# Optimization experiments

Hardware: AMD Instinct MI355X
Metric: run time of the kernel (lower is better)

The kernel has to match this reference:

```python
import jax, jax.numpy as jnp
import numpy as np

N, IN_DIM, OUT_DIM, H = 1024, 128, 128, 4
D = OUT_DIM // H  # head_dim = 32
NEG_SLOPE = 0.2
MASK_VAL = -1e9
LN_EPS = 1e-5


def setup_inputs() -> dict:
    key = jax.random.key(0)
    k = jax.random.split(key, 8)
    h = jax.random.normal(k[0], (N, IN_DIM), dtype=jnp.float32)
    adj = jax.random.randint(k[1], (N, N), 0, 2, dtype=jnp.int32)
    adj = adj.at[jnp.arange(N), jnp.arange(N)].set(1)  # self-loops
    s = 1.0 / np.sqrt(IN_DIM)
    W_l = jax.random.normal(k[2], (IN_DIM, OUT_DIM), dtype=jnp.float32) * s
    W_r = jax.random.normal(k[3], (IN_DIM, OUT_DIM), dtype=jnp.float32) * s
    W_v = jax.random.normal(k[4], (IN_DIM, OUT_DIM), dtype=jnp.float32) * s
    a = jax.random.normal(k[5], (D,), dtype=jnp.float32) * (1.0 / np.sqrt(D))
    ln_g = jnp.ones((OUT_DIM,), dtype=jnp.float32)
    ln_b = jnp.zeros((OUT_DIM,), dtype=jnp.float32)
    return {"h": h, "adj": adj, "W_l": W_l, "W_r": W_r, "W_v": W_v,
            "a": a, "ln_g": ln_g, "ln_b": ln_b}


def reference(h, adj, W_l, W_r, W_v, a, ln_g, ln_b):
    n = h.shape[0]
    Wlh = (h @ W_l).reshape(n, H, D)   # [N,H,D]
    Wrh = (h @ W_r).reshape(n, H, D)   # [N,H,D]
    # pairwise additive scores: pair[i,j,h,d] = Wlh[i] + Wrh[j]
    pair = Wlh[:, None, :, :] + Wrh[None, :, :, :]          # [N,N,H,D]
    pair = jnp.where(pair >= 0, pair, NEG_SLOPE * pair)      # leaky_relu(0.2)
    e = jnp.einsum('ijhd,d->ijh', pair, a)                   # [N,N,H]
    mask = (adj != 0)[:, :, None]                            # [N,N,1]
    e = jnp.where(mask, e, MASK_VAL)
    alpha = jax.nn.softmax(e, axis=1)                        # softmax over j
    v = (h @ W_v).reshape(n, H, D)                           # [N,H,D]
    agg = jnp.einsum('ijh,jhd->ihd', alpha, v).reshape(n, OUT_DIM)
    mu = jnp.mean(agg, axis=-1, keepdims=True)
    var = jnp.mean((agg - mu) ** 2, axis=-1, keepdims=True)
    y = (agg - mu) * jax.lax.rsqrt(var + LN_EPS) * ln_g + ln_b
    return jax.nn.relu(y)
```

## Files before the change

kernel.cpp:

```cpp
#include <hip/hip_runtime.h>
#include <cstdint>

typedef _Float16 f16;
typedef _Float16 f16x2 __attribute__((ext_vector_type(2)));
typedef _Float16 f16x4 __attribute__((ext_vector_type(4)));
typedef _Float16 f16x8 __attribute__((ext_vector_type(8)));
typedef float    f32x4 __attribute__((ext_vector_type(4)));
typedef unsigned short u16;
typedef unsigned int   u32;

#define LOG2E 1.44269504088896340736f

__device__ __forceinline__ f16x2 habs2(f16x2 v) {
    union { f16x2 h; u32 u; } x; x.h = v; x.u &= 0x7FFF7FFFu; return x.h;
}
#if __has_builtin(__builtin_amdgcn_fdot2)
__device__ __forceinline__ float fdot2f(f16x2 a, f16x2 b, float c) {
    return __builtin_amdgcn_fdot2(a, b, c, false);
}
#else
__device__ __forceinline__ float fdot2f(f16x2 a, f16x2 b, float c) {
    return c + (float)a.x * (float)b.x + (float)a.y * (float)b.y;
}
#endif
#if __has_builtin(__builtin_amdgcn_exp2f)
#define EXP2F __builtin_amdgcn_exp2f
#else
#define EXP2F exp2f
#endif

__global__ __launch_bounds__(384) void k1_proj(
        const float* __restrict__ Wl, const float* __restrict__ Wr,
        const float* __restrict__ Wv, const float* __restrict__ h,
        const float* __restrict__ a_,
        f16* __restrict__ Wlh, f16* __restrict__ WrL, f16* __restrict__ VL,
        float* __restrict__ AL, float* __restrict__ BR) {
    __shared__ __align__(16) f16 hS[4][128];
    const int t    = threadIdx.x;
    const int i0   = blockIdx.x * 4;
    const int wsel = t >> 7, col = t & 127;
    const int lane = t & 63;

    for (int e = t; e < 512; e += 384)
        ((f16*)hS)[e] = (f16)h[i0 * 128 + e];

    const float* W = (wsel == 0) ? Wl : ((wsel == 1) ? Wr : Wv);
    f16x2 w2[64];
    #pragma unroll
    for (int c2 = 0; c2 < 64; c2++) {
        f16x2 v;
        v.x = (f16)W[(2 * c2) * 128 + col];
        v.y = (f16)W[(2 * c2 + 1) * 128 + col];
        w2[c2] = v;
    }
    const float asc = 0.6f * a_[col & 31];
    __syncthreads();

    #pragma unroll
    for (int i = 0; i < 4; i++) {
        const int j = i0 + i;
        const f16x2* hr = (const f16x2*)hS[i];
        float acc = 0.f;
        #pragma unroll
        for (int c2 = 0; c2 < 64; c2++) acc = fdot2f(hr[c2], w2[c2], acc);
        const f16 hv = (f16)acc;
        const int hh = col >> 5, dd = col & 31;
        if (wsel == 0) {
            Wlh[j * 128 + col] = hv;
        } else if (wsel == 1) {
            WrL[((hh * 8 + (dd >> 2)) * 1024 + j) * 4 + (dd & 3)] = hv;
        } else {
            VL[(hh * 32 + dd) * 1024 + j] = hv;
        }
        if (wsel < 2) {
            float part = asc * acc;
            #pragma unroll
            for (int off = 1; off < 32; off <<= 1) part += __shfl_xor(part, off);
            if ((lane & 31) == 0) {
                if (wsel == 0) AL[j * 4 + hh] = part;
                else           BR[hh * 1024 + j] = part;
            }
        }
    }
}

__global__ __launch_bounds__(512) void GATv2Layer_84447646974220_kernel(
        const f16* __restrict__ Wlh, const f16* __restrict__ WrL,
        const f16* __restrict__ VL,  const int* __restrict__ adj,
        const float* __restrict__ AL, const float* __restrict__ BR,
        const float* __restrict__ a_, const float* __restrict__ ln_g,
        const float* __restrict__ ln_b, float* __restrict__ out) {

    __shared__ __align__(16) f16 ep[4][4][1024];
    __shared__ float aggS[2][4][128];
    __shared__ float redM[2][4][4];
    __shared__ float redS[2][4][4];

    const int t    = threadIdx.x;
    const int w    = t >> 6;
    const int lane = t & 63;
    const int hh   = w & 3;
    const int half = w >> 2;
    const int i0   = blockIdx.x * 4;

    f16x2 q2[16];
    #pragma unroll
    for (int d2 = 0; d2 < 16; d2++) {
        f16x2 q; q.x = (f16)(0.4f * a_[2 * d2]); q.y = (f16)(0.4f * a_[2 * d2 + 1]);
        q2[d2] = q;
    }
    f16x2 wl2[4][16];
    float al[4];
    #pragma unroll
    for (int ii = 0; ii < 4; ii++) {
        const f16x2* src = (const f16x2*)(Wlh + (i0 + ii) * 128 + hh * 32);
        #pragma unroll
        for (int c2 = 0; c2 < 16; c2++) wl2[ii][c2] = src[c2];
        al[ii] = AL[(i0 + ii) * 4 + hh];
    }

    float maxE[4];
    #pragma unroll
    for (int ii = 0; ii < 4; ii++) maxE[ii] = -__builtin_inff();

    auto LD = [&](int jb, f16x4 (&wr)[8], int (&am)[4], float &bj) {
        int j = half * 512 + jb * 64 + lane;
        #pragma unroll
        for (int c = 0; c < 8; c++)
            wr[c] = *(const f16x4*)(WrL + ((hh * 8 + c) * 1024 + j) * 4);
        #pragma unroll
        for (int ii = 0; ii < 4; ii++) am[ii] = adj[(i0 + ii) * 1024 + j];
        bj = BR[hh * 1024 + j];
    };
    auto CMP = [&](int jb, const f16x4 (&wr)[8], const int (&am)[4], float bj) {
        int j = half * 512 + jb * 64 + lane;
        float e[4];
        #pragma unroll
        for (int ii = 0; ii < 4; ii++) e[ii] = al[ii];
        #pragma unroll
        for (int c = 0; c < 8; c++) {
            #pragma unroll
            for (int ii = 0; ii < 4; ii++) {
                f16x2 t0 = wl2[ii][2 * c]     + wr[c].lo;
                f16x2 t1 = wl2[ii][2 * c + 1] + wr[c].hi;
                e[ii] = fdot2f(q2[2 * c],     habs2(t0), e[ii]);
                e[ii] = fdot2f(q2[2 * c + 1], habs2(t1), e[ii]);
            }
        }
        #pragma unroll
        for (int ii = 0; ii < 4; ii++) {
            float v = am[ii] ? (e[ii] + bj) : -__builtin_inff();
            maxE[ii] = fmaxf(maxE[ii], v);
            ep[hh][ii][j] = (f16)v;
        }
    };

    f16x4 wrA[8], wrB[8];
    int   amA[4], amB[4];
    float bjA, bjB;

    LD(0, wrA, amA, bjA);
    #pragma unroll 1
    for (int jb = 0; jb < 8; jb += 2) {
        LD(jb + 1, wrB, amB, bjB);
        CMP(jb, wrA, amA, bjA);
        if (jb + 2 < 8) LD(jb + 2, wrA, amA, bjA);
        CMP(jb + 1, wrB, amB, bjB);
    }

    #pragma unroll
    for (int ii = 0; ii < 4; ii++) {
        float M = maxE[ii];
        #pragma unroll
        for (int off = 32; off > 0; off >>= 1) M = fmaxf(M, __shfl_xor(M, off));
        if (lane == 0) redM[half][hh][ii] = M;
    }
    __syncthreads();

    #pragma unroll
    for (int ii = 0; ii < 4; ii++) {
        float M = fmaxf(redM[0][hh][ii], redM[1][hh][ii]);
        f16x8 v0 = *(f16x8*)&ep[hh][ii][half * 512 + lane * 8];
        float pb[8], l = 0.f;
        #pragma unroll
        for (int e = 0; e < 8; e++) pb[e] = EXP2F(((float)v0[e] - M) * LOG2E);
        #pragma unroll
        for (int e = 0; e < 8; e++) { v0[e] = (f16)pb[e]; l += pb[e]; }
        *(f16x8*)&ep[hh][ii][half * 512 + lane * 8] = v0;
        #pragma unroll
        for (int off = 32; off > 0; off >>= 1) l += __shfl_xor(l, off);
        if (lane == 0) redS[half][hh][ii] = l;
    }
    __syncthreads();

    float lr[4];
    #pragma unroll
    for (int ii = 0; ii < 4; ii++)
        lr[ii] = 1.0f / (redS[0][hh][ii] + redS[1][hh][ii]);

    f32x4 acc0 = {0.f, 0.f, 0.f, 0.f}, acc1 = {0.f, 0.f, 0.f, 0.f};
    const int q8  = (lane >> 4) << 3;
    const int m3  = lane & 3;
    const int n15 = lane & 15;

    #pragma unroll 2
    for (int jt4 = 0; jt4 < 4; jt4++) {
        int jt = half * 4 + jt4;
        #pragma unroll
        for (int kk = 0; kk < 4; kk++) {
            int ko = jt * 128 + kk * 32 + q8;
            f16x8 af = *(const f16x8*)&ep[hh][m3][ko];
            f16x8 b0 = *(const f16x8*)(VL + (hh * 32 + n15) * 1024 + ko);
            f16x8 b1 = *(const f16x8*)(VL + (hh * 32 + 16 + n15) * 1024 + ko);
            acc0 = __builtin_amdgcn_mfma_f32_16x16x32_f16(af, b0, acc0, 0, 0, 0);
            acc1 = __builtin_amdgcn_mfma_f32_16x16x32_f16(af, b1, acc1, 0, 0, 0);
        }
    }

    if (lane < 16) {
        #pragma unroll
        for (int r = 0; r < 4; r++) {
            aggS[half][r][hh * 32 + lane]      = acc0[r] * lr[r];
            aggS[half][r][hh * 32 + 16 + lane] = acc1[r] * lr[r];
        }
    }
    __syncthreads();

    if (w < 4) {
        float x0 = aggS[0][w][lane]      + aggS[1][w][lane];
        float x1 = aggS[0][w][lane + 64] + aggS[1][w][lane + 64];
        float s = x0 + x1, sq = x0 * x0 + x1 * x1;
        #pragma unroll
        for (int off = 32; off > 0; off >>= 1) {
            s  += __shfl_xor(s, off);
            sq += __shfl_xor(sq, off);
        }
        float mean = s * (1.f / 128.f);
        float var  = sq * (1.f / 128.f) - mean * mean;
        float rs   = rsqrtf(var + 1e-5f);
        float y0 = fmaxf((x0 - mean) * rs * ln_g[lane]      + ln_b[lane],      0.f);
        float y1 = fmaxf((x1 - mean) * rs * ln_g[lane + 64] + ln_b[lane + 64], 0.f);
        out[(i0 + w) * 128 + lane]      = y0;
        out[(i0 + w) * 128 + 64 + lane] = y1;
    }
}

extern "C" void kernel_launch(void* const* d_in, const int* in_sizes, int n_in,
                              void* d_out, int out_size, void* d_ws, size_t ws_size,
                              hipStream_t stream) {
    const float* h   = (const float*)d_in[0];
    const int*   adj = (const int*)d_in[1];
    const float* Wl  = (const float*)d_in[2];
    const float* Wr  = (const float*)d_in[3];
    const float* Wv  = (const float*)d_in[4];
    const float* a_  = (const float*)d_in[5];
    const float* g_  = (const float*)d_in[6];
    const float* b_  = (const float*)d_in[7];
    float* out = (float*)d_out;

    char* ws = (char*)d_ws;
    f16*   Wlh = (f16*)(ws);
    f16*   WrL = (f16*)(ws + 262144);
    f16*   VL  = (f16*)(ws + 524288);
    float* AL  = (float*)(ws + 786432);
    float* BR  = (float*)(ws + 802816);

    k1_proj<<<256, 384, 0, stream>>>(Wl, Wr, Wv, h, a_, Wlh, WrL, VL, AL, BR);
    GATv2Layer_84447646974220_kernel<<<256, 512, 0, stream>>>(
        Wlh, WrL, VL, adj, AL, BR, a_, g_, b_, out);
}
```

Baseline: 95.18 us.

## Precompute adjacency bitmask in LDS and use split-softmax rescaling to drop barrier

The adjacency rows for the block are loaded once up front and compressed into 64-bit ballot masks in shared memory. Before, each of the 8 waves (one per head and half) re-read the same int32 adjacency values inside the score loop. The cross-half max barrier is also removed: each half exponentiates against its own local max, and the two halves are merged after the single remaining barrier by rescaling their partial sums, flash-softmax style. This cuts global loads and one synchronisation but adds an extra barrier at the start and a few exp2 operations. Each half's scaling factor is folded into lr, so the final normalisation stays correct.

```diff
diff --git a/kernel.cpp b/kernel.cpp
--- a/kernel.cpp
+++ b/kernel.cpp
@@ -8,6 +8,7 @@
 typedef float    f32x4 __attribute__((ext_vector_type(4)));
 typedef unsigned short u16;
 typedef unsigned int   u32;
+typedef unsigned long long u64;
 
 #define LOG2E 1.44269504088896340736f
 
@@ -95,6 +96,7 @@
     __shared__ float aggS[2][4][128];
     __shared__ float redM[2][4][4];
     __shared__ float redS[2][4][4];
+    __shared__ u64 amaskS[4][16];
 
     const int t    = threadIdx.x;
     const int w    = t >> 6;
@@ -103,6 +105,17 @@
     const int half = w >> 2;
     const int i0   = blockIdx.x * 4;
 
+    {
+        const int r  = w & 3;
+        const int w0 = (w >> 2) * 8;
+        #pragma unroll
+        for (int c = 0; c < 8; c++) {
+            int av = adj[(i0 + r) * 1024 + (w0 + c) * 64 + lane];
+            u64 m = __ballot(av != 0);
+            if (lane == 0) amaskS[r][w0 + c] = m;
+        }
+    }
+
     f16x2 q2[16];
     #pragma unroll
     for (int d2 = 0; d2 < 16; d2++) {
@@ -118,21 +131,20 @@
         for (int c2 = 0; c2 < 16; c2++) wl2[ii][c2] = src[c2];
         al[ii] = AL[(i0 + ii) * 4 + hh];
     }
+    __syncthreads();
 
     float maxE[4];
     #pragma unroll
     for (int ii = 0; ii < 4; ii++) maxE[ii] = -__builtin_inff();
 
-    auto LD = [&](int jb, f16x4 (&wr)[8], int (&am)[4], float &bj) {
+    auto LD = [&](int jb, f16x4 (&wr)[8], float &bj) {
         int j = half * 512 + jb * 64 + lane;
         #pragma unroll
         for (int c = 0; c < 8; c++)
             wr[c] = *(const f16x4*)(WrL + ((hh * 8 + c) * 1024 + j) * 4);
-        #pragma unroll
-        for (int ii = 0; ii < 4; ii++) am[ii] = adj[(i0 + ii) * 1024 + j];
         bj = BR[hh * 1024 + j];
     };
-    auto CMP = [&](int jb, const f16x4 (&wr)[8], const int (&am)[4], float bj) {
+    auto CMP = [&](int jb, const f16x4 (&wr)[8], float bj) {
         int j = half * 512 + jb * 64 + lane;
         float e[4];
         #pragma unroll
@@ -149,23 +161,23 @@
         }
         #pragma unroll
         for (int ii = 0; ii < 4; ii++) {
-            float v = am[ii] ? (e[ii] + bj) : -__builtin_inff();
+            bool ok = (amaskS[ii][half * 8 + jb] >> lane) & 1ull;
+            float v = ok ? (e[ii] + bj) : -__builtin_inff();
             maxE[ii] = fmaxf(maxE[ii], v);
             ep[hh][ii][j] = (f16)v;
         }
     };
 
     f16x4 wrA[8], wrB[8];
-    int   amA[4], amB[4];
     float bjA, bjB;
 
-    LD(0, wrA, amA, bjA);
+    LD(0, wrA, bjA);
     #pragma unroll 1
     for (int jb = 0; jb < 8; jb += 2) {
-        LD(jb + 1, wrB, amB, bjB);
-        CMP(jb, wrA, amA, bjA);
-        if (jb + 2 < 8) LD(jb + 2, wrA, amA, bjA);
-        CMP(jb + 1, wrB, amB, bjB);
+        LD(jb + 1, wrB, bjB);
+        CMP(jb, wrA, bjA);
+        if (jb + 2 < 8) LD(jb + 2, wrA, bjA);
+        CMP(jb + 1, wrB, bjB);
     }
 
     #pragma unroll
@@ -173,30 +185,34 @@
         float M = maxE[ii];
         #pragma unroll
         for (int off = 32; off > 0; off >>= 1) M = fmaxf(M, __shfl_xor(M, off));
-        if (lane == 0) redM[half][hh][ii] = M;
-    }
-    __syncthreads();
-
-    #pragma unroll
-    for (int ii = 0; ii < 4; ii++) {
-        float M = fmaxf(redM[0][hh][ii], redM[1][hh][ii]);
+        maxE[ii] = M;
+    }
+    #pragma unroll
+    for (int ii = 0; ii < 4; ii++) {
+        float Mk = fmaxf(maxE[ii], -3.0e38f);
         f16x8 v0 = *(f16x8*)&ep[hh][ii][half * 512 + lane * 8];
         float pb[8], l = 0.f;
         #pragma unroll
-        for (int e = 0; e < 8; e++) pb[e] = EXP2F(((float)v0[e] - M) * LOG2E);
+        for (int e = 0; e < 8; e++) pb[e] = EXP2F(((float)v0[e] - Mk) * LOG2E);
         #pragma unroll
         for (int e = 0; e < 8; e++) { v0[e] = (f16)pb[e]; l += pb[e]; }
         *(f16x8*)&ep[hh][ii][half * 512 + lane * 8] = v0;
         #pragma unroll
         for (int off = 32; off > 0; off >>= 1) l += __shfl_xor(l, off);
-        if (lane == 0) redS[half][hh][ii] = l;
+        if (lane == 0) { redM[half][hh][ii] = maxE[ii]; redS[half][hh][ii] = l; }
     }
     __syncthreads();
 
     float lr[4];
     #pragma unroll
-    for (int ii = 0; ii < 4; ii++)
-        lr[ii] = 1.0f / (redS[0][hh][ii] + redS[1][hh][ii]);
+    for (int ii = 0; ii < 4; ii++) {
+        float M0 = redM[0][hh][ii], M1 = redM[1][hh][ii];
+        float M  = fmaxf(M0, M1);
+        float s0 = EXP2F((M0 - M) * LOG2E);
+        float s1 = EXP2F((M1 - M) * LOG2E);
+        float l  = redS[0][hh][ii] * s0 + redS[1][hh][ii] * s1;
+        lr[ii] = (half == 0 ? s0 : s1) / l;
+    }
 
     f32x4 acc0 = {0.f, 0.f, 0.f, 0.f}, acc1 = {0.f, 0.f, 0.f, 0.f};
     const int q8  = (lane >> 4) << 3;
```

After: 97.95 us. 2.9% more time.
